# Performance work log

Measured on AMD Instinct MI355X. Metric: run time of the kernel, lower is better.

## Reference

```python
import jax, jax.numpy as jnp
import numpy as np

H = 128  # hidden_size


def _run_lstm(x, Wx, Wh, b):
    """Unidirectional LSTM over x:(B,T,F). Returns (hs:(B,T,H), c_final:(B,H)).
    Matches flax nn.LSTMCell: gates [i,f,g,o]; input dense has no bias,
    hidden dense has bias b; carry=(c,h), carry[0]=c."""
    B, T, _ = x.shape
    # Hoist the input projection out of the scan: one big GEMM.
    xp = jnp.einsum('btf,fg->tbg', x, Wx) + b  # (T,B,4H)

    def step(carry, gx):
        c, h = carry
        g = gx + h @ Wh  # (B,4H)
        i = jax.nn.sigmoid(g[:, :H])
        f = jax.nn.sigmoid(g[:, H:2 * H])
        gg = jnp.tanh(g[:, 2 * H:3 * H])
        o = jax.nn.sigmoid(g[:, 3 * H:])
        c_new = f * c + i * gg
        h_new = o * jnp.tanh(c_new)
        return (c_new, h_new), h_new

    init = (jnp.zeros((B, H), x.dtype), jnp.zeros((B, H), x.dtype))
    (c_fin, _h_fin), hs = jax.lax.scan(step, init, xp)
    return jnp.swapaxes(hs, 0, 1), c_fin


def _forward(x, params):
    # params: list of (Wx_f, Wh_f, b_f, Wx_b, Wh_b, b_b) per layer
    for li, (Wxf, Whf, bf, Wxb, Whb, bb) in enumerate(params):
        out_f, c_f = _run_lstm(x, Wxf, Whf, bf)
        out_b_rev, c_b = _run_lstm(jnp.flip(x, axis=1), Wxb, Whb, bb)
        out_b = jnp.flip(out_b_rev, axis=1)
        x = jnp.concatenate([out_f, out_b], axis=-1)
        # dropout is identity in eval mode (deterministic reference)
    # NOTE: original code takes carry[0], which in flax LSTMCell is the CELL state.
    h_final = jnp.concatenate([c_f, c_b], axis=-1)
    return x, h_final


def setup_inputs() -> dict:
    key = jax.random.key(0)
    ks = jax.random.split(key, 16)
    B, T, F = 32, 2048, 128
    d = {'x': jax.random.normal(ks[0], (B, T, F), jnp.float32)}
    shapes = {
        'Wx_f0': (F, 4 * H), 'Wh_f0': (H, 4 * H),
        'Wx_b0': (F, 4 * H), 'Wh_b0': (H, 4 * H),
        'Wx_f1': (2 * H, 4 * H), 'Wh_f1': (H, 4 * H),
        'Wx_b1': (2 * H, 4 * H), 'Wh_b1': (H, 4 * H),
    }
    for i, (name, shp) in enumerate(shapes.items()):
        scale = 1.0 / np.sqrt(shp[0])
        d[name] = jax.random.normal(ks[i + 1], shp, jnp.float32) * scale
    for name in ['b_f0', 'b_b0', 'b_f1', 'b_b1']:
        d[name] = jnp.zeros((4 * H,), jnp.float32)
    return d


def reference(x, Wx_f0, Wh_f0, b_f0, Wx_b0, Wh_b0, b_b0,
              Wx_f1, Wh_f1, b_f1, Wx_b1, Wh_b1, b_b1):
    params = [(Wx_f0, Wh_f0, b_f0, Wx_b0, Wh_b0, b_b0),
              (Wx_f1, Wh_f1, b_f1, Wx_b1, Wh_b1, b_b1)]
    return _forward(x, params)
```

## Files before the change

kernel.cpp:

```cpp
#include <hip/hip_runtime.h>
#include <hip/hip_bf16.h>
#include <stdint.h>
#include <type_traits>


#define DEVINL __device__ __forceinline__

typedef __attribute__((ext_vector_type(8))) short short8;
typedef __attribute__((ext_vector_type(4))) float f32x4;

static constexpr int T = 2048;
static constexpr size_t XOUT = (size_t)32 * T * 256;
static constexpr float L2E = 1.4426950408889634f;
static constexpr float M2L2E = -2.8853900817779268f;

DEVINL unsigned short f2bf(float f) {
  unsigned int u = __float_as_uint(f);
  u += 0x7FFFu + ((u >> 16) & 1u);
  return (unsigned short)(u >> 16);
}
DEVINL float gate_scale(int g) { return (g == 2) ? M2L2E : -L2E; }

__global__ __launch_bounds__(256) void prep_wx(const float* wxf0, const float* wxb0,
                                               const float* wxf1, const float* wxb1,
                                               unsigned short* sw0, unsigned short* sw1) {
  int idx = blockIdx.x * 256 + threadIdx.x;
  if (idx < 2 * 65536) {
    int d = idx >> 16;
    int local = idx & 65535;
    const float* w = d ? wxb0 : wxf0;
    int e = local & 7, lane = (local >> 3) & 63, ks = (local >> 9) & 3, ng = local >> 11;
    int col = ng * 16 + (lane & 15);
    int k = ks * 32 + ((lane >> 4) << 3) + e;
    sw0[idx] = f2bf(w[k * 512 + col] * gate_scale(ng >> 3));
  } else {
    int j = idx - 2 * 65536;
    if (j < 2 * 131072) {
      int d = j >> 17;
      int local = j & 131071;
      const float* w = d ? wxb1 : wxf1;
      int e = local & 7, lane = (local >> 3) & 63, ks = (local >> 9) & 7, ng = local >> 12;
      int col = ng * 16 + (lane & 15);
      int k = ks * 32 + ((lane >> 4) << 3) + e;
      sw1[j] = f2bf(w[k * 512 + col] * gate_scale(ng >> 3));
    }
  }
}

__global__ __launch_bounds__(256) void prep_wh(const float* whf0, const float* whb0,
                                               const float* whf1, const float* whb1,
                                               unsigned short* swh) {
  int idx = blockIdx.x * 256 + threadIdx.x;
  if (idx >= 262144) return;
  int e = idx & 7, lane = (idx >> 3) & 63, wid = (idx >> 9) & 7;
  int ks = (idx >> 12) & 3, g = (idx >> 14) & 3, dir = (idx >> 16) & 1, layer = (idx >> 17) & 1;
  const float* w = layer ? (dir ? whb1 : whf1) : (dir ? whb0 : whf0);
  int col = g * 128 + wid * 16 + (lane & 15);
  int k = ks * 32 + ((lane >> 4) << 3) + e;
  swh[idx] = f2bf(w[k * 512 + col] * gate_scale(g));
}

template <int LAYER, bool XPF32>
__global__ __launch_bounds__(256) void input_proj(const float* x, const unsigned short* a_bf,
                                                  const unsigned short* wsw,
                                                  const float* bias_f, const float* bias_b,
                                                  void* xp_out) {
  constexpr int KS = (LAYER == 0) ? 4 : 8;
  int t = blockIdx.x, dir = blockIdx.y;
  int wid = threadIdx.x >> 6, lane = threadIdx.x & 63;
  int p = lane >> 4, c15 = lane & 15;
  const unsigned short* wbase = wsw + (size_t)dir * (32 * KS * 64 * 8);
  const float* bias = dir ? bias_b : bias_f;

  short8 afrag[2][KS];
#pragma unroll
  for (int mt = 0; mt < 2; ++mt) {
#pragma unroll
    for (int ks = 0; ks < KS; ++ks) {
      int m = c15 + mt * 16;
      int kk = ks * 32 + (p << 3);
      if constexpr (LAYER == 0) {
        const float* ap = x + (size_t)m * (T * 128) + (size_t)t * 128 + kk;
        float4 lov = *(const float4*)ap;
        float4 hiv = *(const float4*)(ap + 4);
        short8 s;
        s[0] = (short)f2bf(lov.x); s[1] = (short)f2bf(lov.y);
        s[2] = (short)f2bf(lov.z); s[3] = (short)f2bf(lov.w);
        s[4] = (short)f2bf(hiv.x); s[5] = (short)f2bf(hiv.y);
        s[6] = (short)f2bf(hiv.z); s[7] = (short)f2bf(hiv.w);
        afrag[mt][ks] = s;
      } else {
        afrag[mt][ks] = *(const short8*)(a_bf + ((size_t)t * 32 + m) * 256 + kk);
      }
    }
  }

#pragma unroll
  for (int ngi = 0; ngi < 8; ++ngi) {
    int ng = wid * 8 + ngi;
    int g = ng >> 3, wd = ng & 7;
    f32x4 acc0 = {0.f, 0.f, 0.f, 0.f};
    f32x4 acc1 = {0.f, 0.f, 0.f, 0.f};
#pragma unroll
    for (int ks = 0; ks < KS; ++ks) {
      short8 b = *(const short8*)(wbase + ((size_t)(ng * KS + ks) * 64 + lane) * 8);
      acc0 = __builtin_amdgcn_mfma_f32_16x16x32_bf16(afrag[0][ks], b, acc0, 0, 0, 0);
      acc1 = __builtin_amdgcn_mfma_f32_16x16x32_bf16(afrag[1][ks], b, acc1, 0, 0, 0);
    }
    float bs = bias[ng * 16 + c15] * gate_scale(g);
    int gcol = wd * 16 + c15;
#pragma unroll
    for (int mt = 0; mt < 2; ++mt) {
      f32x4 v = (mt == 0) ? acc0 : acc1;
      v[0] += bs; v[1] += bs; v[2] += bs; v[3] += bs;
      size_t base = (size_t)t * 16384 + (size_t)((mt * 4 + p) * 2048 + gcol * 4 + g);
      if constexpr (XPF32) {
        float* xpf = (float*)xp_out + (size_t)dir * ((size_t)T * 16384);
#pragma unroll
        for (int r = 0; r < 4; ++r) xpf[base + r * 512] = v[r];
      } else {
        unsigned short* xpb = (unsigned short*)xp_out + (size_t)dir * ((size_t)T * 16384);
#pragma unroll
        for (int r = 0; r < 4; ++r) xpb[base + r * 512] = f2bf(v[r]);
      }
    }
  }
}

DEVINL f32x4 gx2v(float4 v) { f32x4 r; r[0]=v.x; r[1]=v.y; r[2]=v.z; r[3]=v.w; return r; }
DEVINL f32x4 gx2v(uint2 u) {
  f32x4 r;
  r[0] = __uint_as_float(u.x << 16);
  r[1] = __uint_as_float(u.x & 0xFFFF0000u);
  r[2] = __uint_as_float(u.y << 16);
  r[3] = __uint_as_float(u.y & 0xFFFF0000u);
  return r;
}

template <int LAYER, bool XPF32>
__global__ __launch_bounds__(512) void lstm_scan(const void* xp, const unsigned short* swh,
                                                 unsigned short* out0, float* dout) {
  using gxT = typename std::conditional<XPF32, float4, uint2>::type;
  int dir = blockIdx.x >> 3;
  int q = blockIdx.x & 7;
  int wid = threadIdx.x >> 6, lane = threadIdx.x & 63;
  int c15 = lane & 15, p = lane >> 4;
  int col = wid * 16 + c15;

  __shared__ __align__(16) unsigned char hA[1280];
  __shared__ __align__(16) unsigned char hB[1280];

  const unsigned short* whbase = swh + (size_t)LAYER * 131072 + (size_t)dir * 65536;
  short8 whf[4][4];
#pragma unroll
  for (int g = 0; g < 4; ++g)
#pragma unroll
    for (int ks = 0; ks < 4; ++ks)
      whf[g][ks] = *(const short8*)(whbase + g * 16384 + ks * 4096 + wid * 512 + lane * 8);

  if (threadIdx.x < 288) {
    ((unsigned int*)hA)[threadIdx.x] = 0u;
    ((unsigned int*)hB)[threadIdx.x] = 0u;
  }

  int aoff[4];
#pragma unroll
  for (int ks = 0; ks < 4; ++ks)
    aoff[ks] = ((lane & 15) >> 2) * 288 + ((lane >> 4) << 4) + ks * 64;
  int woff = p * 288 + col * 2;

  const gxT* gxp = (const gxT*)xp + (size_t)dir * ((size_t)T * 4096);
  int og = q * 512 + p * 128 + col;

  int b = q * 4 + p;
  float cs = 0.f;

  int t0 = dir ? (T - 1) : 0;
  int ts = dir ? -1 : 1;

  gxp += (size_t)t0 * 4096;
  unsigned short* outp_u = out0 + (size_t)t0 * 8192;
  float* dp_u = dout + (size_t)t0 * 256;
  unsigned int oidx = (unsigned int)(b * 256 + dir * 128 + col);
  unsigned int didx = (unsigned int)((size_t)b * T * 256 + dir * 128 + col);
  const ptrdiff_t GXS = (ptrdiff_t)ts * 4096;
  const ptrdiff_t OUS = (ptrdiff_t)ts * 8192;
  const ptrdiff_t DPS = (ptrdiff_t)ts * 256;

  gxT ga = gxp[og];
  gxT gb;
  __syncthreads();

#define STEP(RD, WR, GC, GN)                                                       \
  {                                                                                \
    short8 af0 = *(const short8*)((const char*)(RD) + aoff[0]);                    \
    short8 af1 = *(const short8*)((const char*)(RD) + aoff[1]);                    \
    short8 af2 = *(const short8*)((const char*)(RD) + aoff[2]);                    \
    short8 af3 = *(const short8*)((const char*)(RD) + aoff[3]);                    \
    const f32x4 zz = {0.f, 0.f, 0.f, 0.f};                                         \
    f32x4 gv = gx2v(GC);                                                           \
                                                                   \
    f32x4 acc0 = __builtin_amdgcn_mfma_f32_16x16x32_bf16(af0, whf[0][0], zz, 0,0,0); \
    acc0 = __builtin_amdgcn_mfma_f32_16x16x32_bf16(af1, whf[0][1], acc0, 0, 0, 0); \
    acc0 = __builtin_amdgcn_mfma_f32_16x16x32_bf16(af2, whf[0][2], acc0, 0, 0, 0); \
    acc0 = __builtin_amdgcn_mfma_f32_16x16x32_bf16(af3, whf[0][3], acc0, 0, 0, 0); \
    float ei = __builtin_amdgcn_exp2f(acc0[0] + gv[0]);                            \
                                                                   \
    f32x4 acc1 = __builtin_amdgcn_mfma_f32_16x16x32_bf16(af0, whf[1][0], zz, 0,0,0); \
    acc1 = __builtin_amdgcn_mfma_f32_16x16x32_bf16(af1, whf[1][1], acc1, 0, 0, 0); \
    acc1 = __builtin_amdgcn_mfma_f32_16x16x32_bf16(af2, whf[1][2], acc1, 0, 0, 0); \
    acc1 = __builtin_amdgcn_mfma_f32_16x16x32_bf16(af3, whf[1][3], acc1, 0, 0, 0); \
    float ef = __builtin_amdgcn_exp2f(acc1[0] + gv[1]);                            \
    gxp += GXS;                                                                    \
    GN = gxp[og];                                                                  \
                                                                   \
    f32x4 acc2 = __builtin_amdgcn_mfma_f32_16x16x32_bf16(af0, whf[2][0], zz, 0,0,0); \
    acc2 = __builtin_amdgcn_mfma_f32_16x16x32_bf16(af1, whf[2][1], acc2, 0, 0, 0); \
    acc2 = __builtin_amdgcn_mfma_f32_16x16x32_bf16(af2, whf[2][2], acc2, 0, 0, 0); \
    acc2 = __builtin_amdgcn_mfma_f32_16x16x32_bf16(af3, whf[2][3], acc2, 0, 0, 0); \
    float eg = __builtin_amdgcn_exp2f(acc2[0] + gv[2]);                            \
                                                                   \
    f32x4 acc3 = __builtin_amdgcn_mfma_f32_16x16x32_bf16(af0, whf[3][0], zz, 0,0,0); \
    acc3 = __builtin_amdgcn_mfma_f32_16x16x32_bf16(af1, whf[3][1], acc3, 0, 0, 0); \
    acc3 = __builtin_amdgcn_mfma_f32_16x16x32_bf16(af2, whf[3][2], acc3, 0, 0, 0); \
    acc3 = __builtin_amdgcn_mfma_f32_16x16x32_bf16(af3, whf[3][3], acc3, 0, 0, 0); \
    float eo = __builtin_amdgcn_exp2f(acc3[0] + gv[3]);                            \
                               \
    float ai = 1.0f + ei, av = 1.0f + ef, ag = 1.0f + eg, sg = 1.0f - eg;          \
    float pp = ai * ag;                                                            \
    float num = __builtin_fmaf(cs, pp, sg * av);                                   \
    float rd = __builtin_amdgcn_rcpf(av * pp);                                     \
    float cn = num * rd;                                                           \
    cs = cn;                                                                       \
    float ec = __builtin_amdgcn_exp2f(M2L2E * cn);                                 \
    float ao = 1.0f + eo, ac = 1.0f + ec, sc = 1.0f - ec;                          \
    float rd2 = __builtin_amdgcn_rcpf(ao * ac);                                    \
    float hv = sc * rd2;                                                           \
    unsigned int pk;                                                               \
    asm("v_cvt_pk_bf16_f32 %0, %1, %2" : "=v"(pk) : "v"(hv), "v"(hv));             \
    unsigned short hb = (unsigned short)pk;                                        \
    *(unsigned short*)((char*)(WR) + woff) = hb;                                   \
    if (LAYER == 0) {                                                              \
      outp_u[oidx] = hb;                                                           \
      outp_u += OUS;                                                               \
    } else {                                                                       \
      dp_u[didx] = hv;                                                             \
      dp_u += DPS;                                                                 \
    }                                                                              \
    asm volatile("s_waitcnt lgkmcnt(0)" ::: "memory");                             \
    __builtin_amdgcn_s_barrier();                                                  \
    asm volatile("" ::: "memory");                                                 \
  }

  for (int s = 0; s < T; s += 4) {
    STEP(hA, hB, ga, gb);
    STEP(hB, hA, gb, ga);
    STEP(hA, hB, ga, gb);
    STEP(hB, hA, gb, ga);
  }
#undef STEP

  if constexpr (LAYER == 1) {
    dout[XOUT + (size_t)b * 256 + dir * 128 + col] = cs;
  }
}

extern "C" void kernel_launch(void* const* d_in, const int* in_sizes, int n_in,
                              void* d_out, int out_size, void* d_ws, size_t ws_size,
                              hipStream_t stream) {
  const float* x    = (const float*)d_in[0];
  const float* wxf0 = (const float*)d_in[1];
  const float* whf0 = (const float*)d_in[2];
  const float* wxb0 = (const float*)d_in[3];
  const float* whb0 = (const float*)d_in[4];
  const float* wxf1 = (const float*)d_in[5];
  const float* whf1 = (const float*)d_in[6];
  const float* wxb1 = (const float*)d_in[7];
  const float* whb1 = (const float*)d_in[8];
  const float* bf0  = (const float*)d_in[9];
  const float* bb0  = (const float*)d_in[10];
  const float* bf1  = (const float*)d_in[11];
  const float* bb1  = (const float*)d_in[12];
  float* dout = (float*)d_out;

  const size_t needF32 = 268435456u + 33554432u + 262144u + 524288u + 524288u;
  bool xpf32 = ws_size >= needF32;
  size_t xpBytes = xpf32 ? 268435456u : 134217728u;
  unsigned char* ws = (unsigned char*)d_ws;
  void* xp = (void*)ws;
  unsigned short* out0 = (unsigned short*)(ws + xpBytes);
  unsigned short* sw0  = (unsigned short*)(ws + xpBytes + 33554432u);
  unsigned short* sw1  = sw0 + 2 * 65536;
  unsigned short* swh  = sw1 + 2 * 131072;

  prep_wx<<<1536, 256, 0, stream>>>(wxf0, wxb0, wxf1, wxb1, sw0, sw1);
  prep_wh<<<1024, 256, 0, stream>>>(whf0, whb0, whf1, whb1, swh);

  if (xpf32) {
    input_proj<0, true><<<dim3(2048, 2), 256, 0, stream>>>(x, nullptr, sw0, bf0, bb0, xp);
    lstm_scan<0, true><<<16, 512, 0, stream>>>(xp, swh, out0, dout);
    input_proj<1, true><<<dim3(2048, 2), 256, 0, stream>>>(nullptr, out0, sw1, bf1, bb1, xp);
    lstm_scan<1, true><<<16, 512, 0, stream>>>(xp, swh, out0, dout);
  } else {
    input_proj<0, false><<<dim3(2048, 2), 256, 0, stream>>>(x, nullptr, sw0, bf0, bb0, xp);
    lstm_scan<0, false><<<16, 512, 0, stream>>>(xp, swh, out0, dout);
    input_proj<1, false><<<dim3(2048, 2), 256, 0, stream>>>(nullptr, out0, sw1, bf1, bb1, xp);
    lstm_scan<1, false><<<16, 512, 0, stream>>>(xp, swh, out0, dout);
  }
}
```

Baseline: 1.781 ms.

## Fold gate input projection into MFMA accumulator and interleave gate MFMA chains

```diff
diff --git a/kernel.cpp b/kernel.cpp
--- a/kernel.cpp
+++ b/kernel.cpp
@@ -127,14 +127,14 @@
   }
 }
 
-DEVINL f32x4 gx2v(float4 v) { f32x4 r; r[0]=v.x; r[1]=v.y; r[2]=v.z; r[3]=v.w; return r; }
-DEVINL f32x4 gx2v(uint2 u) {
-  f32x4 r;
-  r[0] = __uint_as_float(u.x << 16);
-  r[1] = __uint_as_float(u.x & 0xFFFF0000u);
-  r[2] = __uint_as_float(u.y << 16);
-  r[3] = __uint_as_float(u.y & 0xFFFF0000u);
-  return r;
+DEVINL void setc(f32x4& c0, f32x4& c1, f32x4& c2, f32x4& c3, float4 v) {
+  c0[0] = v.x; c1[0] = v.y; c2[0] = v.z; c3[0] = v.w;
+}
+DEVINL void setc(f32x4& c0, f32x4& c1, f32x4& c2, f32x4& c3, uint2 u) {
+  c0[0] = __uint_as_float(u.x << 16);
+  c1[0] = __uint_as_float(u.x & 0xFFFF0000u);
+  c2[0] = __uint_as_float(u.y << 16);
+  c3[0] = __uint_as_float(u.y & 0xFFFF0000u);
 }
 
 template <int LAYER, bool XPF32>
@@ -187,45 +187,48 @@
   const ptrdiff_t OUS = (ptrdiff_t)ts * 8192;
   const ptrdiff_t DPS = (ptrdiff_t)ts * 256;
 
+  f32x4 cq0 = {0.f, 0.f, 0.f, 0.f};
+  f32x4 cq1 = {0.f, 0.f, 0.f, 0.f};
+  f32x4 cq2 = {0.f, 0.f, 0.f, 0.f};
+  f32x4 cq3 = {0.f, 0.f, 0.f, 0.f};
+
   gxT ga = gxp[og];
   gxT gb;
   __syncthreads();
 
 #define STEP(RD, WR, GC, GN)                                                       \
   {                                                                                \
+    gxp += GXS;                                                                    \
+    GN = gxp[og];                      \
     short8 af0 = *(const short8*)((const char*)(RD) + aoff[0]);                    \
     short8 af1 = *(const short8*)((const char*)(RD) + aoff[1]);                    \
     short8 af2 = *(const short8*)((const char*)(RD) + aoff[2]);                    \
     short8 af3 = *(const short8*)((const char*)(RD) + aoff[3]);                    \
-    const f32x4 zz = {0.f, 0.f, 0.f, 0.f};                                         \
-    f32x4 gv = gx2v(GC);                                                           \
-                                                                   \
-    f32x4 acc0 = __builtin_amdgcn_mfma_f32_16x16x32_bf16(af0, whf[0][0], zz, 0,0,0); \
+    setc(cq0, cq1, cq2, cq3, GC);              \
+            \
+    f32x4 acc0 = __builtin_amdgcn_mfma_f32_16x16x32_bf16(af0, whf[0][0], cq0, 0,0,0); \
+    f32x4 acc1 = __builtin_amdgcn_mfma_f32_16x16x32_bf16(af0, whf[1][0], cq1, 0,0,0); \
+    f32x4 acc2 = __builtin_amdgcn_mfma_f32_16x16x32_bf16(af0, whf[2][0], cq2, 0,0,0); \
+    f32x4 acc3 = __builtin_amdgcn_mfma_f32_16x16x32_bf16(af0, whf[3][0], cq3, 0,0,0); \
+             \
+                                 \
     acc0 = __builtin_amdgcn_mfma_f32_16x16x32_bf16(af1, whf[0][1], acc0, 0, 0, 0); \
     acc0 = __builtin_amdgcn_mfma_f32_16x16x32_bf16(af2, whf[0][2], acc0, 0, 0, 0); \
     acc0 = __builtin_amdgcn_mfma_f32_16x16x32_bf16(af3, whf[0][3], acc0, 0, 0, 0); \
-    float ei = __builtin_amdgcn_exp2f(acc0[0] + gv[0]);                            \
-                                                                   \
-    f32x4 acc1 = __builtin_amdgcn_mfma_f32_16x16x32_bf16(af0, whf[1][0], zz, 0,0,0); \
+    float ei = __builtin_amdgcn_exp2f(acc0[0]);                                    \
     acc1 = __builtin_amdgcn_mfma_f32_16x16x32_bf16(af1, whf[1][1], acc1, 0, 0, 0); \
     acc1 = __builtin_amdgcn_mfma_f32_16x16x32_bf16(af2, whf[1][2], acc1, 0, 0, 0); \
     acc1 = __builtin_amdgcn_mfma_f32_16x16x32_bf16(af3, whf[1][3], acc1, 0, 0, 0); \
-    float ef = __builtin_amdgcn_exp2f(acc1[0] + gv[1]);                            \
-    gxp += GXS;                                                                    \
-    GN = gxp[og];                                                                  \
-                                                                   \
-    f32x4 acc2 = __builtin_amdgcn_mfma_f32_16x16x32_bf16(af0, whf[2][0], zz, 0,0,0); \
+    float ef = __builtin_amdgcn_exp2f(acc1[0]);                                    \
     acc2 = __builtin_amdgcn_mfma_f32_16x16x32_bf16(af1, whf[2][1], acc2, 0, 0, 0); \
     acc2 = __builtin_amdgcn_mfma_f32_16x16x32_bf16(af2, whf[2][2], acc2, 0, 0, 0); \
     acc2 = __builtin_amdgcn_mfma_f32_16x16x32_bf16(af3, whf[2][3], acc2, 0, 0, 0); \
-    float eg = __builtin_amdgcn_exp2f(acc2[0] + gv[2]);                            \
-                                                                   \
-    f32x4 acc3 = __builtin_amdgcn_mfma_f32_16x16x32_bf16(af0, whf[3][0], zz, 0,0,0); \
+    float eg = __builtin_amdgcn_exp2f(acc2[0]);                                    \
     acc3 = __builtin_amdgcn_mfma_f32_16x16x32_bf16(af1, whf[3][1], acc3, 0, 0, 0); \
     acc3 = __builtin_amdgcn_mfma_f32_16x16x32_bf16(af2, whf[3][2], acc3, 0, 0, 0); \
     acc3 = __builtin_amdgcn_mfma_f32_16x16x32_bf16(af3, whf[3][3], acc3, 0, 0, 0); \
-    float eo = __builtin_amdgcn_exp2f(acc3[0] + gv[3]);                            \
-                               \
+    float eo = __builtin_amdgcn_exp2f(acc3[0]);                                    \
+                 \
     float ai = 1.0f + ei, av = 1.0f + ef, ag = 1.0f + eg, sg = 1.0f - eg;          \
     float pp = ai * ag;                                                            \
     float num = __builtin_fmaf(cs, pp, sg * av);                                   \
```

Measured after the change: 2.288 ms. +28.5%, slower.

## Split LSTM scan into 32 blocks of 4 waves, two batch rows each

Applied to the files above, without the earlier changes.

```diff
diff --git a/kernel.cpp b/kernel.cpp
--- a/kernel.cpp
+++ b/kernel.cpp
@@ -138,27 +138,32 @@
 }
 
 template <int LAYER, bool XPF32>
-__global__ __launch_bounds__(512) void lstm_scan(const void* xp, const unsigned short* swh,
+__global__ __launch_bounds__(256) void lstm_scan(const void* xp, const unsigned short* swh,
                                                  unsigned short* out0, float* dout) {
   using gxT = typename std::conditional<XPF32, float4, uint2>::type;
-  int dir = blockIdx.x >> 3;
-  int q = blockIdx.x & 7;
+  int dir = blockIdx.x >> 4;
+  int qq = blockIdx.x & 15;
   int wid = threadIdx.x >> 6, lane = threadIdx.x & 63;
   int c15 = lane & 15, p = lane >> 4;
-  int col = wid * 16 + c15;
-
-  __shared__ __align__(16) unsigned char hA[1280];
-  __shared__ __align__(16) unsigned char hB[1280];
+  int ngsel = p & 1;
+  int row = p >> 1;
+  int col = wid * 32 + ngsel * 16 + c15;
+
+  __shared__ __align__(16) unsigned char hA[576];
+  __shared__ __align__(16) unsigned char hB[576];
 
   const unsigned short* whbase = swh + (size_t)LAYER * 131072 + (size_t)dir * 65536;
-  short8 whf[4][4];
+  short8 whf[4][2][4];
 #pragma unroll
   for (int g = 0; g < 4; ++g)
 #pragma unroll
-    for (int ks = 0; ks < 4; ++ks)
-      whf[g][ks] = *(const short8*)(whbase + g * 16384 + ks * 4096 + wid * 512 + lane * 8);
-
-  if (threadIdx.x < 288) {
+    for (int n = 0; n < 2; ++n)
+#pragma unroll
+      for (int ks = 0; ks < 4; ++ks)
+        whf[g][n][ks] = *(const short8*)(whbase + g * 16384 + ks * 4096 +
+                                         (wid * 2 + n) * 512 + lane * 8);
+
+  if (threadIdx.x < 144) {
     ((unsigned int*)hA)[threadIdx.x] = 0u;
     ((unsigned int*)hB)[threadIdx.x] = 0u;
   }
@@ -166,13 +171,13 @@
   int aoff[4];
 #pragma unroll
   for (int ks = 0; ks < 4; ++ks)
-    aoff[ks] = ((lane & 15) >> 2) * 288 + ((lane >> 4) << 4) + ks * 64;
-  int woff = p * 288 + col * 2;
-
+    aoff[ks] = ((lane & 15) >> 3) * 288 + (p << 4) + ks * 64;
+  int woff = row * 288 + col * 2;
+
+  int b = qq * 2 + row;
   const gxT* gxp = (const gxT*)xp + (size_t)dir * ((size_t)T * 4096);
-  int og = q * 512 + p * 128 + col;
-
-  int b = q * 4 + p;
+  int og = b * 128 + col;
+
   float cs = 0.f;
 
   int t0 = dir ? (T - 1) : 0;
@@ -199,32 +204,48 @@
     short8 af3 = *(const short8*)((const char*)(RD) + aoff[3]);                    \
     const f32x4 zz = {0.f, 0.f, 0.f, 0.f};                                         \
     f32x4 gv = gx2v(GC);                                                           \
+                                                    \
+    f32x4 a00 = __builtin_amdgcn_mfma_f32_16x16x32_bf16(af0, whf[0][0][0], zz, 0,0,0); \
+    f32x4 a01 = __builtin_amdgcn_mfma_f32_16x16x32_bf16(af0, whf[0][1][0], zz, 0,0,0); \
+    a00 = __builtin_amdgcn_mfma_f32_16x16x32_bf16(af1, whf[0][0][1], a00, 0,0,0);  \
+    a01 = __builtin_amdgcn_mfma_f32_16x16x32_bf16(af1, whf[0][1][1], a01, 0,0,0);  \
+    a00 = __builtin_amdgcn_mfma_f32_16x16x32_bf16(af2, whf[0][0][2], a00, 0,0,0);  \
+    a01 = __builtin_amdgcn_mfma_f32_16x16x32_bf16(af2, whf[0][1][2], a01, 0,0,0);  \
+    a00 = __builtin_amdgcn_mfma_f32_16x16x32_bf16(af3, whf[0][0][3], a00, 0,0,0);  \
+    a01 = __builtin_amdgcn_mfma_f32_16x16x32_bf16(af3, whf[0][1][3], a01, 0,0,0);  \
+    float ei = __builtin_amdgcn_exp2f((ngsel ? a01[0] : a00[0]) + gv[0]);          \
                                                                    \
-    f32x4 acc0 = __builtin_amdgcn_mfma_f32_16x16x32_bf16(af0, whf[0][0], zz, 0,0,0); \
-    acc0 = __builtin_amdgcn_mfma_f32_16x16x32_bf16(af1, whf[0][1], acc0, 0, 0, 0); \
-    acc0 = __builtin_amdgcn_mfma_f32_16x16x32_bf16(af2, whf[0][2], acc0, 0, 0, 0); \
-    acc0 = __builtin_amdgcn_mfma_f32_16x16x32_bf16(af3, whf[0][3], acc0, 0, 0, 0); \
-    float ei = __builtin_amdgcn_exp2f(acc0[0] + gv[0]);                            \
-                                                                   \
-    f32x4 acc1 = __builtin_amdgcn_mfma_f32_16x16x32_bf16(af0, whf[1][0], zz, 0,0,0); \
-    acc1 = __builtin_amdgcn_mfma_f32_16x16x32_bf16(af1, whf[1][1], acc1, 0, 0, 0); \
-    acc1 = __builtin_amdgcn_mfma_f32_16x16x32_bf16(af2, whf[1][2], acc1, 0, 0, 0); \
-    acc1 = __builtin_amdgcn_mfma_f32_16x16x32_bf16(af3, whf[1][3], acc1, 0, 0, 0); \
-    float ef = __builtin_amdgcn_exp2f(acc1[0] + gv[1]);                            \
+    f32x4 a10 = __builtin_amdgcn_mfma_f32_16x16x32_bf16(af0, whf[1][0][0], zz, 0,0,0); \
+    f32x4 a11 = __builtin_amdgcn_mfma_f32_16x16x32_bf16(af0, whf[1][1][0], zz, 0,0,0); \
+    a10 = __builtin_amdgcn_mfma_f32_16x16x32_bf16(af1, whf[1][0][1], a10, 0,0,0);  \
+    a11 = __builtin_amdgcn_mfma_f32_16x16x32_bf16(af1, whf[1][1][1], a11, 0,0,0);  \
+    a10 = __builtin_amdgcn_mfma_f32_16x16x32_bf16(af2, whf[1][0][2], a10, 0,0,0);  \
+    a11 = __builtin_amdgcn_mfma_f32_16x16x32_bf16(af2, whf[1][1][2], a11, 0,0,0);  \
+    a10 = __builtin_amdgcn_mfma_f32_16x16x32_bf16(af3, whf[1][0][3], a10, 0,0,0);  \
+    a11 = __builtin_amdgcn_mfma_f32_16x16x32_bf16(af3, whf[1][1][3], a11, 0,0,0);  \
+    float ef = __builtin_amdgcn_exp2f((ngsel ? a11[0] : a10[0]) + gv[1]);          \
     gxp += GXS;                                                                    \
     GN = gxp[og];                                                                  \
                                                                    \
-    f32x4 acc2 = __builtin_amdgcn_mfma_f32_16x16x32_bf16(af0, whf[2][0], zz, 0,0,0); \
-    acc2 = __builtin_amdgcn_mfma_f32_16x16x32_bf16(af1, whf[2][1], acc2, 0, 0, 0); \
-    acc2 = __builtin_amdgcn_mfma_f32_16x16x32_bf16(af2, whf[2][2], acc2, 0, 0, 0); \
-    acc2 = __builtin_amdgcn_mfma_f32_16x16x32_bf16(af3, whf[2][3], acc2, 0, 0, 0); \
-    float eg = __builtin_amdgcn_exp2f(acc2[0] + gv[2]);                            \
+    f32x4 a20 = __builtin_amdgcn_mfma_f32_16x16x32_bf16(af0, whf[2][0][0], zz, 0,0,0); \
+    f32x4 a21 = __builtin_amdgcn_mfma_f32_16x16x32_bf16(af0, whf[2][1][0], zz, 0,0,0); \
+    a20 = __builtin_amdgcn_mfma_f32_16x16x32_bf16(af1, whf[2][0][1], a20, 0,0,0);  \
+    a21 = __builtin_amdgcn_mfma_f32_16x16x32_bf16(af1, whf[2][1][1], a21, 0,0,0);  \
+    a20 = __builtin_amdgcn_mfma_f32_16x16x32_bf16(af2, whf[2][0][2], a20, 0,0,0);  \
+    a21 = __builtin_amdgcn_mfma_f32_16x16x32_bf16(af2, whf[2][1][2], a21, 0,0,0);  \
+    a20 = __builtin_amdgcn_mfma_f32_16x16x32_bf16(af3, whf[2][0][3], a20, 0,0,0);  \
+    a21 = __builtin_amdgcn_mfma_f32_16x16x32_bf16(af3, whf[2][1][3], a21, 0,0,0);  \
+    float eg = __builtin_amdgcn_exp2f((ngsel ? a21[0] : a20[0]) + gv[2]);          \
                                                                    \
-    f32x4 acc3 = __builtin_amdgcn_mfma_f32_16x16x32_bf16(af0, whf[3][0], zz, 0,0,0); \
-    acc3 = __builtin_amdgcn_mfma_f32_16x16x32_bf16(af1, whf[3][1], acc3, 0, 0, 0); \
-    acc3 = __builtin_amdgcn_mfma_f32_16x16x32_bf16(af2, whf[3][2], acc3, 0, 0, 0); \
-    acc3 = __builtin_amdgcn_mfma_f32_16x16x32_bf16(af3, whf[3][3], acc3, 0, 0, 0); \
-    float eo = __builtin_amdgcn_exp2f(acc3[0] + gv[3]);                            \
+    f32x4 a30 = __builtin_amdgcn_mfma_f32_16x16x32_bf16(af0, whf[3][0][0], zz, 0,0,0); \
+    f32x4 a31 = __builtin_amdgcn_mfma_f32_16x16x32_bf16(af0, whf[3][1][0], zz, 0,0,0); \
+    a30 = __builtin_amdgcn_mfma_f32_16x16x32_bf16(af1, whf[3][0][1], a30, 0,0,0);  \
+    a31 = __builtin_amdgcn_mfma_f32_16x16x32_bf16(af1, whf[3][1][1], a31, 0,0,0);  \
+    a30 = __builtin_amdgcn_mfma_f32_16x16x32_bf16(af2, whf[3][0][2], a30, 0,0,0);  \
+    a31 = __builtin_amdgcn_mfma_f32_16x16x32_bf16(af2, whf[3][1][2], a31, 0,0,0);  \
+    a30 = __builtin_amdgcn_mfma_f32_16x16x32_bf16(af3, whf[3][0][3], a30, 0,0,0);  \
+    a31 = __builtin_amdgcn_mfma_f32_16x16x32_bf16(af3, whf[3][1][3], a31, 0,0,0);  \
+    float eo = __builtin_amdgcn_exp2f((ngsel ? a31[0] : a30[0]) + gv[3]);          \
                                \
     float ai = 1.0f + ei, av = 1.0f + ef, ag = 1.0f + eg, sg = 1.0f - eg;          \
     float pp = ai * ag;                                                            \
@@ -298,13 +319,13 @@
 
   if (xpf32) {
     input_proj<0, true><<<dim3(2048, 2), 256, 0, stream>>>(x, nullptr, sw0, bf0, bb0, xp);
-    lstm_scan<0, true><<<16, 512, 0, stream>>>(xp, swh, out0, dout);
+    lstm_scan<0, true><<<32, 256, 0, stream>>>(xp, swh, out0, dout);
     input_proj<1, true><<<dim3(2048, 2), 256, 0, stream>>>(nullptr, out0, sw1, bf1, bb1, xp);
-    lstm_scan<1, true><<<16, 512, 0, stream>>>(xp, swh, out0, dout);
+    lstm_scan<1, true><<<32, 256, 0, stream>>>(xp, swh, out0, dout);
   } else {
     input_proj<0, false><<<dim3(2048, 2), 256, 0, stream>>>(x, nullptr, sw0, bf0, bb0, xp);
-    lstm_scan<0, false><<<16, 512, 0, stream>>>(xp, swh, out0, dout);
+    lstm_scan<0, false><<<32, 256, 0, stream>>>(xp, swh, out0, dout);
     input_proj<1, false><<<dim3(2048, 2), 256, 0, stream>>>(nullptr, out0, sw1, bf1, bb1, xp);
-    lstm_scan<1, false><<<16, 512, 0, stream>>>(xp, swh, out0, dout);
-  }
-}
+    lstm_scan<1, false><<<32, 256, 0, stream>>>(xp, swh, out0, dout);
+  }
+}
```

Result: slower. 2.028 ms (+13.9%).
